# Performance work log

Hardware: AMD Instinct MI355X
Metric: run time of the kernel (lower is better)

## Reference

```python
import jax, jax.numpy as jnp
import numpy as np

B, L, H, N2, NLAYERS = 8, 4096, 256, 32, 4


def setup_inputs() -> dict:
    key = jax.random.key(0)
    ks = jax.random.split(key, 7)
    x = jax.random.normal(ks[0], (B, L, H), dtype=jnp.float32)
    # S4D kernel params (per layer, stacked on leading dim)
    dt_min, dt_max = 1e-3, 1e-1
    u = jax.random.uniform(ks[1], (NLAYERS, H), dtype=jnp.float32)
    log_dt = u * (np.log(dt_max) - np.log(dt_min)) + np.log(dt_min)
    log_A_real = jnp.log(0.5 * jnp.ones((NLAYERS, H, N2), jnp.float32))
    A_imag = jnp.broadcast_to(np.pi * jnp.arange(N2, dtype=jnp.float32), (NLAYERS, H, N2)) * jnp.ones((NLAYERS, H, N2), jnp.float32)
    C_re = jax.random.normal(ks[2], (NLAYERS, H, N2), dtype=jnp.float32) * (0.5 ** 0.5)
    C_im = jax.random.normal(ks[3], (NLAYERS, H, N2), dtype=jnp.float32) * (0.5 ** 0.5)
    D = jax.random.normal(ks[4], (NLAYERS, H), dtype=jnp.float32)
    Wout = jax.random.normal(ks[5], (NLAYERS, 2 * H, H), dtype=jnp.float32) * (1.0 / H) ** 0.5
    bout = jnp.zeros((NLAYERS, 2 * H), jnp.float32)
    ln_g = jnp.ones((NLAYERS, H), jnp.float32)
    ln_b = jnp.zeros((NLAYERS, H), jnp.float32)
    return dict(x=x, log_dt=log_dt, log_A_real=log_A_real, A_imag=A_imag,
                C_re=C_re, C_im=C_im, D=D, Wout=Wout, bout=bout,
                ln_g=ln_g, ln_b=ln_b)


def _s4d_kernel(log_dt, log_A_real, A_imag, C_re, C_im, Lseq):
    # Vandermonde kernel of S4D: k[h,l] = 2*Re sum_n C'_hn exp(dt_h*A_hn*l)
    dt = jnp.exp(log_dt)                       # (H,)
    A = (-jnp.exp(log_A_real) + 1j * A_imag)   # (H,N) complex
    C = C_re + 1j * C_im                       # (H,N)
    dtA = A * dt[:, None]                      # (H,N)
    K = jnp.exp(dtA[:, :, None] * jnp.arange(Lseq, dtype=jnp.float32))  # (H,N,L)
    Cm = C * (jnp.exp(dtA) - 1.0) / A          # ZOH discretization of C
    return 2.0 * jnp.einsum('hn,hnl->hl', Cm, K).real  # (H,L)


def _s4d_layer(u, log_dt, log_A_real, A_imag, C_re, C_im, D, Wout, bout):
    # u: (B,H,L)
    Lq = u.shape[-1]
    k = _s4d_kernel(log_dt, log_A_real, A_imag, C_re, C_im, Lq)  # (H,L)
    kf = jnp.fft.rfft(k, n=2 * Lq)             # (H, L+1)
    uf = jnp.fft.rfft(u, n=2 * Lq)             # (B,H,L+1)
    y = jnp.fft.irfft(uf * kf, n=2 * Lq)[..., :Lq]
    y = y + u * D[:, None]
    y = jax.nn.gelu(y, approximate=False)
    # output linear: 1x1 conv H->2H followed by GLU along channel dim
    y = jnp.einsum('oh,bhl->bol', Wout, y) + bout[None, :, None]
    a, b = jnp.split(y, 2, axis=1)
    return a * jax.nn.sigmoid(b)               # (B,H,L)


def _layernorm_ch(x, g, b, eps=1e-5):
    # x: (B,H,L); normalize over channel axis H (matches norm on (B,L,H))
    m = jnp.mean(x, axis=1, keepdims=True)
    v = jnp.mean((x - m) ** 2, axis=1, keepdims=True)
    return (x - m) / jnp.sqrt(v + eps) * g[None, :, None] + b[None, :, None]


def reference(x, log_dt, log_A_real, A_imag, C_re, C_im, D, Wout, bout, ln_g, ln_b):
    u = jnp.swapaxes(x, -1, -2)  # (B,H,L)
    for i in range(NLAYERS):  # post-norm (prenorm=False), dropout=identity (eval)
        z = _s4d_layer(u, log_dt[i], log_A_real[i], A_imag[i], C_re[i], C_im[i],
                       D[i], Wout[i], bout[i])
        u = z + u
        u = _layernorm_ch(u, ln_g[i], ln_b[i])
    return jnp.swapaxes(u, -1, -2)  # (B,L,H)
```

## Files before the change

### kernel.cpp

```cpp
#include <hip/hip_runtime.h>
#include <math.h>

#define B    8
#define L    4096
#define H    256
#define N2   32
#define NL   4
#define O2   512
#define BLK  64
#define NBLK 64
#define TVP  136
#define MJP  72
#define UTP  72
#define INP  68
#define TL2  64
#define YPAD 264
#define URP  72

typedef __attribute__((ext_vector_type(8))) short short8;
typedef __attribute__((ext_vector_type(4))) float f32x4;

__device__ __forceinline__ unsigned short f2bf(float f)
{
    unsigned int u = __float_as_uint(f);
    unsigned int r = (u + 0x7fffu + ((u >> 16) & 1u)) >> 16;
    return (unsigned short)r;
}

__device__ __forceinline__ float bf2f(unsigned short v)
{
    return __uint_as_float(((unsigned int)v) << 16);
}

__device__ __forceinline__ float gelu_f(float x)
{
    float t = 1.59576912161f * fmaf(0.044715f * x * x, x, x);
    return x / (1.f + __expf(-t));
}

__global__ __launch_bounds__(256) void k_setup(
    const float* __restrict__ x, const float* __restrict__ log_dt,
    const float* __restrict__ log_Ar, const float* __restrict__ A_im,
    const float* __restrict__ C_re, const float* __restrict__ C_im,
    const float* __restrict__ Dv, const float* __restrict__ Wout,
    unsigned short* __restrict__ Wb, unsigned short* __restrict__ TVc,
    unsigned short* __restrict__ Mm, float2* __restrict__ w64c,
    unsigned short* __restrict__ u)
{
    __shared__ __align__(16) unsigned char smem_raw[27648];
    const int bid = blockIdx.x;
    const int t = threadIdx.x;

    if (bid < 512) {
        int idx = (bid * 256 + t) * 4;
        float4 v = *(const float4*)(Wout + idx);
        ushort4 o;
        o.x = f2bf(v.x); o.y = f2bf(v.y); o.z = f2bf(v.z); o.w = f2bf(v.w);
        *(ushort4*)(Wb + idx) = o;
    } else if (bid < 1536) {
        unsigned short* tvS = (unsigned short*)smem_raw;
        unsigned short* mmS = tvS + BLK * TVP;
        float* kbS = (float*)(mmS + BLK * MJP);
        float* cS  = kbS + BLK;
        const int id = bid - 512;
        const int layer = id >> 8, h = id & 255;
        if (t < 32) {
            const int n0 = t;
            const int idx = (layer * H + h) * N2 + n0;
            double dt = exp((double)log_dt[layer * H + h]);
            double Ar = -exp((double)log_Ar[idx]);
            double Ai = (double)A_im[idx];
            double dtr = dt * Ar, dti = dt * Ai;
            double er = exp(dtr);
            double dwr = er * cos(dti), dwi = er * sin(dti);
            double numr = dwr - 1.0, numi = dwi;
            double den = Ar * Ar + Ai * Ai;
            double qr0 = (numr * Ar + numi * Ai) / den;
            double qi0 = (numi * Ar - numr * Ai) / den;
            double dcr = (double)C_re[idx], dci = (double)C_im[idx];
            cS[n0]       = (float)(2.0 * (dcr * qr0 - dci * qi0));
            cS[32 + n0]  = (float)(2.0 * (dcr * qi0 + dci * qr0));
            cS[64 + n0]  = (float)dwr;
            cS[96 + n0]  = (float)dwi;
            double rev = dti * 0.15915494309189535;
            cS[128 + n0] = (float)(rev - floor(rev));
            cS[160 + n0] = (float)dtr;
            double m64 = exp(64.0 * dtr);
            double a64 = 64.0 * dti;
            w64c[(layer * H + h) * N2 + n0] =
                make_float2((float)(m64 * cos(a64)), (float)(m64 * sin(a64)));
        }
        __syncthreads();
        const int n = t & 31, dg = t >> 5;
        const float cr = cS[n], ci = cS[32 + n];
        const float wr = cS[64 + n], wi = cS[96 + n];
        const float revf = cS[128 + n], dtrf = cS[160 + n];
#pragma unroll
        for (int i = 0; i < 8; ++i) {
            const int d = dg * 8 + i;
            float ph = (float)d * revf;
            ph = (ph - floorf(ph)) * 6.28318530718f;
            float mag = __expf((float)d * dtrf);
            float vr = mag * __cosf(ph);
            float vi = mag * __sinf(ph);
            float pk = fmaf(cr, vr, -(ci * vi));
            pk += __shfl_xor(pk, 1);  pk += __shfl_xor(pk, 2);
            pk += __shfl_xor(pk, 4);  pk += __shfl_xor(pk, 8);
            pk += __shfl_xor(pk, 16);
            if (n == 0) kbS[d] = pk;
            mmS[n * MJP + (63 - d)]        = f2bf(vr);
            mmS[(32 + n) * MJP + (63 - d)] = f2bf(vi);
            float v1r = vr * wr - vi * wi;
            float v1i = vr * wi + vi * wr;
            tvS[d * TVP + 64 + n] = f2bf(fmaf(cr, v1r, -(ci * v1i)));
            tvS[d * TVP + 96 + n] = f2bf(-fmaf(cr, v1i, ci * v1r));
        }
        __syncthreads();
        {
            const int r = t >> 2, c0 = (t & 3) * 16;
            const float diag = kbS[0] + Dv[layer * H + h];
            short8 o8[2];
#pragma unroll
            for (int j = 0; j < 16; ++j) {
                int c = c0 + j;
                float val = (c > r) ? 0.f : ((c == r) ? diag : kbS[r - c]);
                o8[j >> 3][j & 7] = (short)f2bf(val);
            }
            *(short8*)&tvS[r * TVP + c0]     = o8[0];
            *(short8*)&tvS[r * TVP + c0 + 8] = o8[1];
        }
        __syncthreads();
        unsigned short* tv = TVc + (size_t)(layer * H + h) * BLK * TVP;
        unsigned short* mm = Mm + (size_t)(layer * H + h) * BLK * MJP;
        for (int c = t; c < (BLK * TVP) / 8; c += 256)
            *(short8*)(tv + c * 8) = *(const short8*)&tvS[c * 8];
        for (int c = t; c < (BLK * MJP) / 8; c += 256)
            *(short8*)(mm + c * 8) = *(const short8*)&mmS[c * 8];
    } else {
        float* sh = (float*)smem_raw;
        const int rb = bid - 1536;
        const int hx = rb & 7, ly = (rb >> 3) & 63, b = rb >> 9;
        const int h0 = hx * 32, l0 = ly * 64;
        const int tx = t & 7, ty = t >> 3;
        const float* xb = x + ((size_t)b * L + l0) * H + h0;
#pragma unroll
        for (int i = 0; i < 2; ++i) {
            int l = ty + i * 32;
            float4 v = *(const float4*)(xb + (size_t)l * H + tx * 4);
            sh[(tx * 4 + 0) * 68 + l] = v.x;
            sh[(tx * 4 + 1) * 68 + l] = v.y;
            sh[(tx * 4 + 2) * 68 + l] = v.z;
            sh[(tx * 4 + 3) * 68 + l] = v.w;
        }
        __syncthreads();
        const int hh = t >> 3, cc = (t & 7) * 8;
        const float* row = &sh[hh * 68 + cc];
        short8 o8;
#pragma unroll
        for (int j = 0; j < 8; ++j) o8[j] = (short)f2bf(row[j]);
        *(short8*)(u + ((size_t)b * H + h0 + hh) * L + l0 + cc) = o8;
    }
}

__global__ __launch_bounds__(256) void k_scan3(
    const unsigned short* __restrict__ u, const unsigned short* __restrict__ Mm_l,
    const unsigned short* __restrict__ TVc_l, const float2* __restrict__ w64c_l,
    unsigned short* __restrict__ y)
{
    __shared__ __align__(16) unsigned short uT[BLK * UTP];
    __shared__ __align__(16) unsigned short ST[BLK * UTP];
    __shared__ __align__(16) float INC[BLK * INP];
    __shared__ float2 cLd[4][32];
    const int t = threadIdx.x;
    const int wv = t >> 6, lane = t & 63;
    const int lanei = lane & 15, quad = lane >> 4;
    const int h = blockIdx.x & 255, ct = blockIdx.x >> 8;
    const unsigned short* ub = u + (size_t)(ct * H + h) * L;

    const unsigned short* arowA = Mm_l + (size_t)h * BLK * MJP + (wv * 16 + lanei) * MJP + quad * 8;
    short8 mA[2];
    mA[0] = *(const short8*)(arowA);
    mA[1] = *(const short8*)(arowA + 32);
    const unsigned short* arowB = TVc_l + (size_t)h * BLK * TVP + (wv * 16 + lanei) * TVP + quad * 8;
    short8 tB[4];
#pragma unroll
    for (int kt = 0; kt < 4; ++kt)
        tB[kt] = *(const short8*)(arowB + kt * 32);
    const float2 w64 = w64c_l[h * N2 + (lane & 31)];

    {
        int col = t >> 2, q = t & 3;
        *(short8*)&uT[col * UTP + q * 16]     = *(const short8*)(ub + col * 64 + q * 16);
        *(short8*)&uT[col * UTP + q * 16 + 8] = *(const short8*)(ub + col * 64 + q * 16 + 8);
    }
    __syncthreads();

    {
        f32x4 acc[4];
#pragma unroll
        for (int nt = 0; nt < 4; ++nt) acc[nt] = (f32x4){0.f, 0.f, 0.f, 0.f};
#pragma unroll
        for (int kt = 0; kt < 2; ++kt) {
#pragma unroll
            for (int nt = 0; nt < 4; ++nt) {
                short8 b8 = *(const short8*)&uT[(nt * 16 + lanei) * UTP + kt * 32 + quad * 8];
                acc[nt] = __builtin_amdgcn_mfma_f32_16x16x32_bf16(mA[kt], b8, acc[nt], 0, 0, 0);
            }
        }
#pragma unroll
        for (int nt = 0; nt < 4; ++nt)
            *(f32x4*)&INC[(nt * 16 + lanei) * INP + wv * 16 + quad * 4] = acc[nt];
    }
    __syncthreads();

    const int n = lane & 31;
    float Pr[16], Pi[16];
    float w1r = 1.f, w1i = 0.f;
    if (lane < 32) {
        float sr = 0.f, si = 0.f;
        const int base = wv * 16;
#pragma unroll
        for (int k = 0; k < 16; ++k) {
            Pr[k] = sr; Pi[k] = si;
            float ir = INC[(base + k) * INP + n];
            float ii = INC[(base + k) * INP + 32 + n];
            float nr = fmaf(w64.x, sr, fmaf(-w64.y, si, ir));
            float ni = fmaf(w64.x, si, fmaf(w64.y, sr, ii));
            sr = nr; si = ni;
        }
        cLd[wv][n] = make_float2(sr, si);
        float ar = w64.x, ai = w64.y;
#pragma unroll
        for (int q = 0; q < 4; ++q) {
            float nr2 = ar * ar - ai * ai;
            float ni2 = 2.f * ar * ai;
            ar = nr2; ai = ni2;
        }
        w1r = ar; w1i = ai;
    }
    __syncthreads();
    if (lane < 32) {
        float Cr = 0.f, Ci = 0.f;
        for (int wp = 0; wp < wv; ++wp) {
            float2 Lw = cLd[wp][n];
            float nr = fmaf(w1r, Cr, fmaf(-w1i, Ci, Lw.x));
            float ni = fmaf(w1r, Ci, fmaf(w1i, Cr, Lw.y));
            Cr = nr; Ci = ni;
        }
        float pr = 1.f, pi = 0.f;
#pragma unroll
        for (int k = 0; k < 16; ++k) {
            int blk = wv * 16 + k;
            float Sr = fmaf(pr, Cr, fmaf(-pi, Ci, Pr[k]));
            float Si = fmaf(pr, Ci, fmaf(pi, Cr, Pi[k]));
            ST[blk * UTP + n]      = f2bf(Sr);
            ST[blk * UTP + 32 + n] = f2bf(Si);
            float npr = pr * w64.x - pi * w64.y;
            float npi = pr * w64.y + pi * w64.x;
            pr = npr; pi = npi;
        }
    }
    __syncthreads();

    {
        f32x4 acc[4];
#pragma unroll
        for (int nt = 0; nt < 4; ++nt) acc[nt] = (f32x4){0.f, 0.f, 0.f, 0.f};
#pragma unroll
        for (int kt = 0; kt < 4; ++kt) {
            const unsigned short* bb = (kt < 2) ? uT : ST;
            int ko = (kt & 1) * 32 + quad * 8;
#pragma unroll
            for (int nt = 0; nt < 4; ++nt) {
                short8 b8 = *(const short8*)&bb[(nt * 16 + lanei) * UTP + ko];
                acc[nt] = __builtin_amdgcn_mfma_f32_16x16x32_bf16(tB[kt], b8, acc[nt], 0, 0, 0);
            }
        }
        __syncthreads();
#pragma unroll
        for (int nt = 0; nt < 4; ++nt) {
            int blk = nt * 16 + lanei;
            int i0 = wv * 16 + quad * 4;
            ushort4 o4;
            o4.x = f2bf(gelu_f(acc[nt][0]));
            o4.y = f2bf(gelu_f(acc[nt][1]));
            o4.z = f2bf(gelu_f(acc[nt][2]));
            o4.w = f2bf(gelu_f(acc[nt][3]));
            *(ushort4*)&uT[blk * UTP + i0] = o4;
        }
        __syncthreads();
        unsigned short* yb = y + (size_t)(ct * H + h) * L;
#pragma unroll
        for (int r = 0; r < 2; ++r) {
            int c = r * 256 + t;
            int o = c >> 3, c8 = (c & 7) * 8;
            *(short8*)(yb + o * 64 + c8) = *(const short8*)&uT[o * UTP + c8];
        }
    }
}

__global__ __launch_bounds__(512, 4) void k_gemm(
    const unsigned short* __restrict__ y, unsigned short* __restrict__ u,
    const unsigned short* __restrict__ Wb, const float* __restrict__ bo,
    const float* __restrict__ lng, const float* __restrict__ lnb,
    float* __restrict__ outp)
{
    __shared__ __align__(16) unsigned short yS[H * URP];
    __shared__ float bS[O2];
    __shared__ float lgS[H], lbS[H];
    __shared__ float redS[8][4][16], redQ[8][4][16];

    const int t = threadIdx.x;
    const int wv = t >> 6;
    const int lane = t & 63;
    const int lanei = lane & 15;
    const int quad = lane >> 4;
    const int b = blockIdx.x >> 6;
    const int l0 = (blockIdx.x & 63) * TL2;

    size_t abase[2][2];
#pragma unroll
    for (int p = 0; p < 2; ++p)
#pragma unroll
        for (int jj = 0; jj < 2; ++jj)
            abase[p][jj] = (size_t)(p * 256 + wv * 32 + jj * 16 + lanei) * H + quad * 8;

    short8 a8p[4];
#pragma unroll
    for (int p = 0; p < 2; ++p)
#pragma unroll
        for (int jj = 0; jj < 2; ++jj)
            a8p[p * 2 + jj] = *(const short8*)(Wb + abase[p][jj]);

    {
        const int i = t & 7, hr = t >> 3;
        const unsigned short* yb = y + (size_t)b * H * L + l0 + i * 8;
#pragma unroll
        for (int ps = 0; ps < 4; ++ps) {
            int h = ps * 64 + hr;
            short8 v8 = *(const short8*)(yb + (size_t)h * L);
#pragma unroll
            for (int r = 0; r < 8; ++r)
                yS[(i * 8 + r) * YPAD + (h ^ (8 * i))] = (unsigned short)v8[r];
        }
        if (t < O2) bS[t] = bo[t];
        if (t < H) { lgS[t] = lng[t]; lbS[t] = lnb[t]; }
    }
    __syncthreads();

    f32x4 acc[2][2][4];
#pragma unroll
    for (int p = 0; p < 2; ++p)
#pragma unroll
        for (int jj = 0; jj < 2; ++jj)
#pragma unroll
            for (int nt = 0; nt < 4; ++nt)
                acc[p][jj][nt] = (f32x4){0.f, 0.f, 0.f, 0.f};

#pragma unroll
    for (int kt = 0; kt < 8; ++kt) {
        short8 a8[4];
        if (kt == 0) {
            a8[0] = a8p[0]; a8[1] = a8p[1]; a8[2] = a8p[2]; a8[3] = a8p[3];
        } else {
#pragma unroll
            for (int q = 0; q < 4; ++q)
                a8[q] = *(const short8*)(Wb + abase[q >> 1][q & 1] + kt * 32);
        }
        short8 bfr[4];
#pragma unroll
        for (int nt = 0; nt < 4; ++nt) {
            int lp = nt * 16 + lanei;
            int a = (2 * nt + (lanei >> 3)) & 7;
            bfr[nt] = *(const short8*)&yS[lp * YPAD + ((kt * 32 + quad * 8) ^ (8 * a))];
        }
#pragma unroll
        for (int p = 0; p < 2; ++p)
#pragma unroll
            for (int jj = 0; jj < 2; ++jj) {
#pragma unroll
                for (int nt = 0; nt < 4; ++nt)
                    acc[p][jj][nt] = __builtin_amdgcn_mfma_f32_16x16x32_bf16(
                        a8[p * 2 + jj], bfr[nt], acc[p][jj][nt], 0, 0, 0);
            }
    }
    __syncthreads();

    unsigned short* ub = u + (size_t)b * H * L + l0;
#pragma unroll
    for (int r = 0; r < 4; ++r) {
        int c = r * 512 + t;
        int o = c >> 3, c8 = (c & 7) * 8;
        *(short8*)&yS[o * URP + c8] = *(const short8*)(ub + (size_t)o * L + c8);
    }
    __syncthreads();

    float psum[4] = {0.f, 0.f, 0.f, 0.f}, psq[4] = {0.f, 0.f, 0.f, 0.f};
#pragma unroll
    for (int jj = 0; jj < 2; ++jj) {
#pragma unroll
        for (int nt = 0; nt < 4; ++nt) {
            int lc = nt * 16 + lanei;
#pragma unroll
            for (int reg = 0; reg < 4; ++reg) {
                int o = wv * 32 + jj * 16 + quad * 4 + reg;
                float a = acc[0][jj][nt][reg] + bS[o];
                float g = acc[1][jj][nt][reg] + bS[o + 256];
                float glu = a / (1.f + __expf(-g));
                float val = glu + bf2f(yS[o * URP + lc]);
                acc[0][jj][nt][reg] = val;
                psum[nt] += val;
                psq[nt] = fmaf(val, val, psq[nt]);
            }
        }
    }
#pragma unroll
    for (int nt = 0; nt < 4; ++nt) {
        psum[nt] += __shfl_xor(psum[nt], 16);
        psum[nt] += __shfl_xor(psum[nt], 32);
        psq[nt]  += __shfl_xor(psq[nt], 16);
        psq[nt]  += __shfl_xor(psq[nt], 32);
    }
    if (lane < 16) {
#pragma unroll
        for (int nt = 0; nt < 4; ++nt) {
            redS[wv][nt][lanei] = psum[nt];
            redQ[wv][nt][lanei] = psq[nt];
        }
    }
    __syncthreads();
    float mcol[4], icol[4];
#pragma unroll
    for (int nt = 0; nt < 4; ++nt) {
        float s = 0.f, q = 0.f;
#pragma unroll
        for (int w = 0; w < 8; ++w) { s += redS[w][nt][lanei]; q += redQ[w][nt][lanei]; }
        float m = s * (1.0f / 256.0f);
        float v = q * (1.0f / 256.0f) - m * m;
        mcol[nt] = m;
        icol[nt] = rsqrtf(v + 1e-5f);
    }
    if (outp == nullptr) {
#pragma unroll
        for (int jj = 0; jj < 2; ++jj) {
#pragma unroll
            for (int nt = 0; nt < 4; ++nt) {
                int lc = nt * 16 + lanei;
#pragma unroll
                for (int reg = 0; reg < 4; ++reg) {
                    int o = wv * 32 + jj * 16 + quad * 4 + reg;
                    float val = acc[0][jj][nt][reg];
                    float ov = (val - mcol[nt]) * icol[nt] * lgS[o] + lbS[o];
                    yS[o * URP + lc] = f2bf(ov);
                }
            }
        }
        __syncthreads();
#pragma unroll
        for (int r = 0; r < 4; ++r) {
            int c = r * 512 + t;
            int o = c >> 3, c8 = (c & 7) * 8;
            *(short8*)(ub + (size_t)o * L + c8) = *(const short8*)&yS[o * URP + c8];
        }
    } else {
#pragma unroll
        for (int jj = 0; jj < 2; ++jj) {
#pragma unroll
            for (int nt = 0; nt < 4; ++nt) {
                int lc = nt * 16 + lanei;
                int o0 = wv * 32 + jj * 16 + quad * 4;
                float4 ov;
#pragma unroll
                for (int reg = 0; reg < 4; ++reg) {
                    int o = o0 + reg;
                    float val = acc[0][jj][nt][reg];
                    ((float*)&ov)[reg] = (val - mcol[nt]) * icol[nt] * lgS[o] + lbS[o];
                }
                *(float4*)(outp + ((size_t)b * L + l0 + lc) * H + o0) = ov;
            }
        }
    }
}

extern "C" void kernel_launch(void* const* d_in, const int* in_sizes, int n_in,
                              void* d_out, int out_size, void* d_ws, size_t ws_size,
                              hipStream_t stream)
{
    const float* x      = (const float*)d_in[0];
    const float* log_dt = (const float*)d_in[1];
    const float* log_Ar = (const float*)d_in[2];
    const float* A_im   = (const float*)d_in[3];
    const float* C_re   = (const float*)d_in[4];
    const float* C_im   = (const float*)d_in[5];
    const float* Dv     = (const float*)d_in[6];
    const float* Wout   = (const float*)d_in[7];
    const float* bout   = (const float*)d_in[8];
    const float* lng    = (const float*)d_in[9];
    const float* lnb    = (const float*)d_in[10];
    float* out = (float*)d_out;

    unsigned short* u   = (unsigned short*)d_ws;
    unsigned short* Wb  = u + (size_t)B * H * L;
    unsigned short* TVc = Wb + (size_t)NL * O2 * H;
    unsigned short* Mm  = TVc + (size_t)NL * H * BLK * TVP;
    float2* w64c        = (float2*)(Mm + (size_t)NL * H * BLK * MJP);
    unsigned short* y   = (unsigned short*)(w64c + (size_t)NL * H * N2);

    k_setup<<<5632, 256, 0, stream>>>(x, log_dt, log_Ar, A_im, C_re, C_im, Dv, Wout,
                                      Wb, TVc, Mm, w64c, u);
    for (int layer = 0; layer < NL; ++layer) {
        k_scan3<<<H * 8, 256, 0, stream>>>(u, Mm + (size_t)layer * H * BLK * MJP,
                                           TVc + (size_t)layer * H * BLK * TVP,
                                           w64c + (size_t)layer * H * N2, y);
        k_gemm<<<B * L / TL2, 512, 0, stream>>>(y, u, Wb + (size_t)layer * O2 * H,
                                                bout + layer * O2, lng + layer * H, lnb + layer * H,
                                                (layer == NL - 1) ? out : nullptr);
    }
}
```

Before: 294.8 us.

## Process two L-tiles per GEMM block to reuse weight fragments

The GEMM+GLU+LayerNorm kernel now handles two 64-column tiles per workgroup (grid halved to 256 blocks), sharing each weight fragment load across both tiles' MFMAs. It also prefetches the residual tile for the second half into registers while the first tile's epilogue runs. This trades lower occupancy (launch bounds 4→2, double LDS, double accumulators) for fewer global weight reads and more MFMA work per load. With 256 blocks, some CUs on the part may sit idle.

```diff
diff --git a/kernel.cpp b/kernel.cpp
--- a/kernel.cpp
+++ b/kernel.cpp
@@ -16,6 +16,7 @@
 #define TL2  64
 #define YPAD 264
 #define URP  72
+#define YSZ  20512
 
 typedef __attribute__((ext_vector_type(8))) short short8;
 typedef __attribute__((ext_vector_type(4))) float f32x4;
@@ -299,13 +300,14 @@
     }
 }
 
-__global__ __launch_bounds__(512, 4) void k_gemm(
+__global__ __launch_bounds__(512, 2) void k_gemm(
     const unsigned short* __restrict__ y, unsigned short* __restrict__ u,
     const unsigned short* __restrict__ Wb, const float* __restrict__ bo,
     const float* __restrict__ lng, const float* __restrict__ lnb,
     float* __restrict__ outp)
 {
-    __shared__ __align__(16) unsigned short yS[H * URP];
+    __shared__ __align__(16) unsigned short ySA[YSZ];
+    __shared__ __align__(16) unsigned short ySB[YSZ];
     __shared__ float bS[O2];
     __shared__ float lgS[H], lbS[H];
     __shared__ float redS[8][4][16], redQ[8][4][16];
@@ -315,8 +317,10 @@
     const int lane = t & 63;
     const int lanei = lane & 15;
     const int quad = lane >> 4;
-    const int b = blockIdx.x >> 6;
-    const int l0 = (blockIdx.x & 63) * TL2;
+    const int idxA = blockIdx.x;
+    const int idxB = blockIdx.x + 256;
+    const int bA = idxA >> 6, l0A = (idxA & 63) * TL2;
+    const int bB = idxB >> 6, l0B = (idxB & 63) * TL2;
 
     size_t abase[2][2];
 #pragma unroll
@@ -325,122 +329,103 @@
         for (int jj = 0; jj < 2; ++jj)
             abase[p][jj] = (size_t)(p * 256 + wv * 32 + jj * 16 + lanei) * H + quad * 8;
 
-    short8 a8p[4];
-#pragma unroll
-    for (int p = 0; p < 2; ++p)
-#pragma unroll
-        for (int jj = 0; jj < 2; ++jj)
-            a8p[p * 2 + jj] = *(const short8*)(Wb + abase[p][jj]);
-
     {
         const int i = t & 7, hr = t >> 3;
-        const unsigned short* yb = y + (size_t)b * H * L + l0 + i * 8;
+        const unsigned short* ybA = y + (size_t)bA * H * L + l0A + i * 8;
+        const unsigned short* ybB = y + (size_t)bB * H * L + l0B + i * 8;
+        short8 vA[4], vB[4];
+#pragma unroll
+        for (int ps = 0; ps < 4; ++ps)
+            vA[ps] = *(const short8*)(ybA + (size_t)(ps * 64 + hr) * L);
+#pragma unroll
+        for (int ps = 0; ps < 4; ++ps)
+            vB[ps] = *(const short8*)(ybB + (size_t)(ps * 64 + hr) * L);
 #pragma unroll
         for (int ps = 0; ps < 4; ++ps) {
             int h = ps * 64 + hr;
-            short8 v8 = *(const short8*)(yb + (size_t)h * L);
 #pragma unroll
             for (int r = 0; r < 8; ++r)
-                yS[(i * 8 + r) * YPAD + (h ^ (8 * i))] = (unsigned short)v8[r];
+                ySA[(i * 8 + r) * YPAD + (h ^ (8 * i))] = (unsigned short)vA[ps][r];
+        }
+#pragma unroll
+        for (int ps = 0; ps < 4; ++ps) {
+            int h = ps * 64 + hr;
+#pragma unroll
+            for (int r = 0; r < 8; ++r)
+                ySB[(i * 8 + r) * YPAD + (h ^ (8 * i))] = (unsigned short)vB[ps][r];
         }
         if (t < O2) bS[t] = bo[t];
         if (t < H) { lgS[t] = lng[t]; lbS[t] = lnb[t]; }
     }
     __syncthreads();
 
-    f32x4 acc[2][2][4];
+    f32x4 accA[2][2][4], accB[2][2][4];
 #pragma unroll
     for (int p = 0; p < 2; ++p)
 #pragma unroll
         for (int jj = 0; jj < 2; ++jj)
 #pragma unroll
-            for (int nt = 0; nt < 4; ++nt)
-                acc[p][jj][nt] = (f32x4){0.f, 0.f, 0.f, 0.f};
+            for (int nt = 0; nt < 4; ++nt) {
+                accA[p][jj][nt] = (f32x4){0.f, 0.f, 0.f, 0.f};
+                accB[p][jj][nt] = (f32x4){0.f, 0.f, 0.f, 0.f};
+            }
 
 #pragma unroll
     for (int kt = 0; kt < 8; ++kt) {
         short8 a8[4];
-        if (kt == 0) {
-            a8[0] = a8p[0]; a8[1] = a8p[1]; a8[2] = a8p[2]; a8[3] = a8p[3];
-        } else {
-#pragma unroll
-            for (int q = 0; q < 4; ++q)
-                a8[q] = *(const short8*)(Wb + abase[q >> 1][q & 1] + kt * 32);
-        }
-        short8 bfr[4];
+#pragma unroll
+        for (int q = 0; q < 4; ++q)
+            a8[q] = *(const short8*)(Wb + abase[q >> 1][q & 1] + kt * 32);
+        short8 bfrA[4], bfrB[4];
 #pragma unroll
         for (int nt = 0; nt < 4; ++nt) {
             int lp = nt * 16 + lanei;
             int a = (2 * nt + (lanei >> 3)) & 7;
-            bfr[nt] = *(const short8*)&yS[lp * YPAD + ((kt * 32 + quad * 8) ^ (8 * a))];
+            int off = lp * YPAD + ((kt * 32 + quad * 8) ^ (8 * a));
+            bfrA[nt] = *(const short8*)&ySA[off];
+            bfrB[nt] = *(const short8*)&ySB[off];
         }
 #pragma unroll
         for (int p = 0; p < 2; ++p)
 #pragma unroll
             for (int jj = 0; jj < 2; ++jj) {
 #pragma unroll
-                for (int nt = 0; nt < 4; ++nt)
-                    acc[p][jj][nt] = __builtin_amdgcn_mfma_f32_16x16x32_bf16(
-                        a8[p * 2 + jj], bfr[nt], acc[p][jj][nt], 0, 0, 0);
-            }
-    }
-    __syncthreads();
-
-    unsigned short* ub = u + (size_t)b * H * L + l0;
+                for (int nt = 0; nt < 4; ++nt) {
+                    accA[p][jj][nt] = __builtin_amdgcn_mfma_f32_16x16x32_bf16(
+                        a8[p * 2 + jj], bfrA[nt], accA[p][jj][nt], 0, 0, 0);
+                    accB[p][jj][nt] = __builtin_amdgcn_mfma_f32_16x16x32_bf16(
+                        a8[p * 2 + jj], bfrB[nt], accB[p][jj][nt], 0, 0, 0);
+                }
+            }
+    }
+
+    unsigned short* ubA = u + (size_t)bA * H * L + l0A;
+    unsigned short* ubB = u + (size_t)bB * H * L + l0B;
+    short8 rA[4];
 #pragma unroll
     for (int r = 0; r < 4; ++r) {
         int c = r * 512 + t;
         int o = c >> 3, c8 = (c & 7) * 8;
-        *(short8*)&yS[o * URP + c8] = *(const short8*)(ub + (size_t)o * L + c8);
-    }
-    __syncthreads();
-
-    float psum[4] = {0.f, 0.f, 0.f, 0.f}, psq[4] = {0.f, 0.f, 0.f, 0.f};
-#pragma unroll
-    for (int jj = 0; jj < 2; ++jj) {
-#pragma unroll
-        for (int nt = 0; nt < 4; ++nt) {
-            int lc = nt * 16 + lanei;
-#pragma unroll
-            for (int reg = 0; reg < 4; ++reg) {
-                int o = wv * 32 + jj * 16 + quad * 4 + reg;
-                float a = acc[0][jj][nt][reg] + bS[o];
-                float g = acc[1][jj][nt][reg] + bS[o + 256];
-                float glu = a / (1.f + __expf(-g));
-                float val = glu + bf2f(yS[o * URP + lc]);
-                acc[0][jj][nt][reg] = val;
-                psum[nt] += val;
-                psq[nt] = fmaf(val, val, psq[nt]);
-            }
-        }
-    }
-#pragma unroll
-    for (int nt = 0; nt < 4; ++nt) {
-        psum[nt] += __shfl_xor(psum[nt], 16);
-        psum[nt] += __shfl_xor(psum[nt], 32);
-        psq[nt]  += __shfl_xor(psq[nt], 16);
-        psq[nt]  += __shfl_xor(psq[nt], 32);
-    }
-    if (lane < 16) {
-#pragma unroll
-        for (int nt = 0; nt < 4; ++nt) {
-            redS[wv][nt][lanei] = psum[nt];
-            redQ[wv][nt][lanei] = psq[nt];
-        }
-    }
-    __syncthreads();
-    float mcol[4], icol[4];
-#pragma unroll
-    for (int nt = 0; nt < 4; ++nt) {
-        float s = 0.f, q = 0.f;
-#pragma unroll
-        for (int w = 0; w < 8; ++w) { s += redS[w][nt][lanei]; q += redQ[w][nt][lanei]; }
-        float m = s * (1.0f / 256.0f);
-        float v = q * (1.0f / 256.0f) - m * m;
-        mcol[nt] = m;
-        icol[nt] = rsqrtf(v + 1e-5f);
-    }
-    if (outp == nullptr) {
+        rA[r] = *(const short8*)(ubA + (size_t)o * L + c8);
+    }
+    __syncthreads();
+#pragma unroll
+    for (int r = 0; r < 4; ++r) {
+        int c = r * 512 + t;
+        int o = c >> 3, c8 = (c & 7) * 8;
+        *(short8*)&ySA[o * URP + c8] = rA[r];
+    }
+    short8 rB[4];
+#pragma unroll
+    for (int r = 0; r < 4; ++r) {
+        int c = r * 512 + t;
+        int o = c >> 3, c8 = (c & 7) * 8;
+        rB[r] = *(const short8*)(ubB + (size_t)o * L + c8);
+    }
+    __syncthreads();
+
+    {
+        float psum[4] = {0.f, 0.f, 0.f, 0.f}, psq[4] = {0.f, 0.f, 0.f, 0.f};
 #pragma unroll
         for (int jj = 0; jj < 2; ++jj) {
 #pragma unroll
@@ -449,34 +434,177 @@
 #pragma unroll
                 for (int reg = 0; reg < 4; ++reg) {
                     int o = wv * 32 + jj * 16 + quad * 4 + reg;
-                    float val = acc[0][jj][nt][reg];
-                    float ov = (val - mcol[nt]) * icol[nt] * lgS[o] + lbS[o];
-                    yS[o * URP + lc] = f2bf(ov);
+                    float a = accA[0][jj][nt][reg] + bS[o];
+                    float g = accA[1][jj][nt][reg] + bS[o + 256];
+                    float glu = a / (1.f + __expf(-g));
+                    float val = glu + bf2f(ySA[o * URP + lc]);
+                    accA[0][jj][nt][reg] = val;
+                    psum[nt] += val;
+                    psq[nt] = fmaf(val, val, psq[nt]);
                 }
             }
         }
-        __syncthreads();
-#pragma unroll
-        for (int r = 0; r < 4; ++r) {
-            int c = r * 512 + t;
-            int o = c >> 3, c8 = (c & 7) * 8;
-            *(short8*)(ub + (size_t)o * L + c8) = *(const short8*)&yS[o * URP + c8];
-        }
-    } else {
+#pragma unroll
+        for (int nt = 0; nt < 4; ++nt) {
+            psum[nt] += __shfl_xor(psum[nt], 16);
+            psum[nt] += __shfl_xor(psum[nt], 32);
+            psq[nt]  += __shfl_xor(psq[nt], 16);
+            psq[nt]  += __shfl_xor(psq[nt], 32);
+        }
+        if (lane < 16) {
+#pragma unroll
+            for (int nt = 0; nt < 4; ++nt) {
+                redS[wv][nt][lanei] = psum[nt];
+                redQ[wv][nt][lanei] = psq[nt];
+            }
+        }
+        __syncthreads();
+        float mcol[4], icol[4];
+#pragma unroll
+        for (int nt = 0; nt < 4; ++nt) {
+            float s = 0.f, q = 0.f;
+#pragma unroll
+            for (int w = 0; w < 8; ++w) { s += redS[w][nt][lanei]; q += redQ[w][nt][lanei]; }
+            float m = s * (1.0f / 256.0f);
+            float v = q * (1.0f / 256.0f) - m * m;
+            mcol[nt] = m;
+            icol[nt] = rsqrtf(v + 1e-5f);
+        }
+        if (outp == nullptr) {
+#pragma unroll
+            for (int jj = 0; jj < 2; ++jj) {
+#pragma unroll
+                for (int nt = 0; nt < 4; ++nt) {
+                    int lc = nt * 16 + lanei;
+#pragma unroll
+                    for (int reg = 0; reg < 4; ++reg) {
+                        int o = wv * 32 + jj * 16 + quad * 4 + reg;
+                        float val = accA[0][jj][nt][reg];
+                        float ov = (val - mcol[nt]) * icol[nt] * lgS[o] + lbS[o];
+                        ySA[o * URP + lc] = f2bf(ov);
+                    }
+                }
+            }
+            __syncthreads();
+#pragma unroll
+            for (int r = 0; r < 4; ++r) {
+                int c = r * 512 + t;
+                int o = c >> 3, c8 = (c & 7) * 8;
+                *(short8*)(ubA + (size_t)o * L + c8) = *(const short8*)&ySA[o * URP + c8];
+            }
+        } else {
+#pragma unroll
+            for (int jj = 0; jj < 2; ++jj) {
+#pragma unroll
+                for (int nt = 0; nt < 4; ++nt) {
+                    int lc = nt * 16 + lanei;
+                    int o0 = wv * 32 + jj * 16 + quad * 4;
+                    float4 ov;
+#pragma unroll
+                    for (int reg = 0; reg < 4; ++reg) {
+                        int o = o0 + reg;
+                        float val = accA[0][jj][nt][reg];
+                        ((float*)&ov)[reg] = (val - mcol[nt]) * icol[nt] * lgS[o] + lbS[o];
+                    }
+                    *(float4*)(outp + ((size_t)bA * L + l0A + lc) * H + o0) = ov;
+                }
+            }
+            __syncthreads();
+        }
+    }
+
+#pragma unroll
+    for (int r = 0; r < 4; ++r) {
+        int c = r * 512 + t;
+        int o = c >> 3, c8 = (c & 7) * 8;
+        *(short8*)&ySB[o * URP + c8] = rB[r];
+    }
+    __syncthreads();
+
+    {
+        float psum[4] = {0.f, 0.f, 0.f, 0.f}, psq[4] = {0.f, 0.f, 0.f, 0.f};
 #pragma unroll
         for (int jj = 0; jj < 2; ++jj) {
 #pragma unroll
             for (int nt = 0; nt < 4; ++nt) {
                 int lc = nt * 16 + lanei;
-                int o0 = wv * 32 + jj * 16 + quad * 4;
-                float4 ov;
 #pragma unroll
                 for (int reg = 0; reg < 4; ++reg) {
-                    int o = o0 + reg;
-                    float val = acc[0][jj][nt][reg];
-                    ((float*)&ov)[reg] = (val - mcol[nt]) * icol[nt] * lgS[o] + lbS[o];
+                    int o = wv * 32 + jj * 16 + quad * 4 + reg;
+                    float a = accB[0][jj][nt][reg] + bS[o];
+                    float g = accB[1][jj][nt][reg] + bS[o + 256];
+                    float glu = a / (1.f + __expf(-g));
+                    float val = glu + bf2f(ySB[o * URP + lc]);
+                    accB[0][jj][nt][reg] = val;
+                    psum[nt] += val;
+                    psq[nt] = fmaf(val, val, psq[nt]);
                 }
-                *(float4*)(outp + ((size_t)b * L + l0 + lc) * H + o0) = ov;
+            }
+        }
+#pragma unroll
+        for (int nt = 0; nt < 4; ++nt) {
+            psum[nt] += __shfl_xor(psum[nt], 16);
+            psum[nt] += __shfl_xor(psum[nt], 32);
+            psq[nt]  += __shfl_xor(psq[nt], 16);
+            psq[nt]  += __shfl_xor(psq[nt], 32);
+        }
+        if (lane < 16) {
+#pragma unroll
+            for (int nt = 0; nt < 4; ++nt) {
+                redS[wv][nt][lanei] = psum[nt];
+                redQ[wv][nt][lanei] = psq[nt];
+            }
+        }
+        __syncthreads();
+        float mcol[4], icol[4];
+#pragma unroll
+        for (int nt = 0; nt < 4; ++nt) {
+            float s = 0.f, q = 0.f;
+#pragma unroll
+            for (int w = 0; w < 8; ++w) { s += redS[w][nt][lanei]; q += redQ[w][nt][lanei]; }
+            float m = s * (1.0f / 256.0f);
+            float v = q * (1.0f / 256.0f) - m * m;
+            mcol[nt] = m;
+            icol[nt] = rsqrtf(v + 1e-5f);
+        }
+        if (outp == nullptr) {
+#pragma unroll
+            for (int jj = 0; jj < 2; ++jj) {
+#pragma unroll
+                for (int nt = 0; nt < 4; ++nt) {
+                    int lc = nt * 16 + lanei;
+#pragma unroll
+                    for (int reg = 0; reg < 4; ++reg) {
+                        int o = wv * 32 + jj * 16 + quad * 4 + reg;
+                        float val = accB[0][jj][nt][reg];
+                        float ov = (val - mcol[nt]) * icol[nt] * lgS[o] + lbS[o];
+                        ySB[o * URP + lc] = f2bf(ov);
+                    }
+                }
+            }
+            __syncthreads();
+#pragma unroll
+            for (int r = 0; r < 4; ++r) {
+                int c = r * 512 + t;
+                int o = c >> 3, c8 = (c & 7) * 8;
+                *(short8*)(ubB + (size_t)o * L + c8) = *(const short8*)&ySB[o * URP + c8];
+            }
+        } else {
+#pragma unroll
+            for (int jj = 0; jj < 2; ++jj) {
+#pragma unroll
+                for (int nt = 0; nt < 4; ++nt) {
+                    int lc = nt * 16 + lanei;
+                    int o0 = wv * 32 + jj * 16 + quad * 4;
+                    float4 ov;
+#pragma unroll
+                    for (int reg = 0; reg < 4; ++reg) {
+                        int o = o0 + reg;
+                        float val = accB[0][jj][nt][reg];
+                        ((float*)&ov)[reg] = (val - mcol[nt]) * icol[nt] * lgS[o] + lbS[o];
+                    }
+                    *(float4*)(outp + ((size_t)bB * L + l0B + lc) * H + o0) = ov;
+                }
             }
         }
     }
@@ -512,8 +640,8 @@
         k_scan3<<<H * 8, 256, 0, stream>>>(u, Mm + (size_t)layer * H * BLK * MJP,
                                            TVc + (size_t)layer * H * BLK * TVP,
                                            w64c + (size_t)layer * H * N2, y);
-        k_gemm<<<B * L / TL2, 512, 0, stream>>>(y, u, Wb + (size_t)layer * O2 * H,
-                                                bout + layer * O2, lng + layer * H, lnb + layer * H,
-                                                (layer == NL - 1) ? out : nullptr);
+        k_gemm<<<256, 512, 0, stream>>>(y, u, Wb + (size_t)layer * O2 * H,
+                                        bout + layer * O2, lng + layer * H, lnb + layer * H,
+                                        (layer == NL - 1) ? out : nullptr);
     }
 }
```

Result: faster. 272.2 us (-7.7%).
